# Performance work log

Measured on AMD Instinct MI355X. Metric: run time of the kernel, lower is better.

## Reference

```python
import jax, jax.numpy as jnp
import numpy as np

B, L, D = 2, 2048, 1024
H, HD = 16, 64   # num_heads, head_dim
LD = 256         # mla latent dim


def setup_inputs() -> dict:
    key = jax.random.key(0)
    ks = jax.random.split(key, 6)
    s = lambda fan_in: 1.0 / np.sqrt(fan_in)
    x_bld = jax.random.normal(ks[0], (B, L, D), dtype=jnp.float32)
    Wq = jax.random.normal(ks[1], (D, H, HD), dtype=jnp.float32) * s(D)
    Wkv_down = jax.random.normal(ks[2], (D, LD), dtype=jnp.float32) * s(D)
    Wk_up = jax.random.normal(ks[3], (LD, H, HD), dtype=jnp.float32) * s(LD)
    Wv_up = jax.random.normal(ks[4], (LD, H, HD), dtype=jnp.float32) * s(LD)
    Wout = jax.random.normal(ks[5], (H, HD, D), dtype=jnp.float32) * s(H * HD)
    return {"x_bld": x_bld, "Wq": Wq, "Wkv_down": Wkv_down,
            "Wk_up": Wk_up, "Wv_up": Wv_up, "Wout": Wout}


def reference(x_bld, Wq, Wkv_down, Wk_up, Wv_up, Wout):
    # projections
    q_blhd = jnp.einsum('bld,dhk->blhk', x_bld, Wq)
    latent_bll = jnp.einsum('bld,dc->blc', x_bld, Wkv_down)   # [B,L,LD]
    k_blhd = jnp.einsum('blc,chk->blhk', latent_bll, Wk_up)
    v_blhd = jnp.einsum('blc,chk->blhk', latent_bll, Wv_up)
    # attention scores [B,H,L,L]
    attn = jnp.einsum('bqhd,bkhd->bhqk', q_blhd, k_blhd) / jnp.sqrt(
        jnp.asarray(HD, dtype=x_bld.dtype))
    # causal mask (no window)
    l = x_bld.shape[1]
    mask = (jnp.arange(l)[None, :] <= jnp.arange(l)[:, None])[None, None]
    neg_inf = jnp.finfo(attn.dtype).min
    attn = jax.nn.softmax(jnp.where(mask, attn, neg_inf), axis=-1)
    y_blhd = jnp.einsum('bhqk,bkhd->bqhd', attn, v_blhd)
    return jnp.einsum('bqhd,hdo->bqo', y_blhd, Wout)
```

## Files before the change

### kernel.cpp

```cpp
#include <hip/hip_runtime.h>
#include <hip/hip_bf16.h>

#define BB   2
#define LL   2048
#define DD   1024
#define HH   16
#define HDD  64
#define LDIM 256
#define MTOT (BB * LL)

using short8  = __attribute__((ext_vector_type(8))) short;
using floatx4 = __attribute__((ext_vector_type(4))) float;

static __device__ __forceinline__ unsigned short f2bf(float x) {
  __hip_bfloat16 h = __float2bfloat16(x);
  return *reinterpret_cast<unsigned short*>(&h);
}
static __device__ __forceinline__ unsigned int pk_bf16(float a, float b) {
  return (unsigned int)f2bf(a) | ((unsigned int)f2bf(b) << 16);
}
static __device__ __forceinline__ void load_lds16(const unsigned short* g,
                                                  unsigned short* l) {
  __builtin_amdgcn_global_load_lds(
      (const __attribute__((address_space(1))) unsigned int*)g,
      (__attribute__((address_space(3))) unsigned int*)l, 16, 0, 0);
}
template <int N>
static __device__ __forceinline__ void waitcnt_vm() {
  if constexpr (N == 0) asm volatile("s_waitcnt vmcnt(0)" ::: "memory");
  else if constexpr (N == 2) asm volatile("s_waitcnt vmcnt(2)" ::: "memory");
  else if constexpr (N == 4) asm volatile("s_waitcnt vmcnt(4)" ::: "memory");
  else if constexpr (N == 6) asm volatile("s_waitcnt vmcnt(6)" ::: "memory");
  else if constexpr (N == 8) asm volatile("s_waitcnt vmcnt(8)" ::: "memory");
}
static __device__ __forceinline__ void lds_drain_barrier() {
  asm volatile("s_waitcnt lgkmcnt(0)\n\ts_barrier" ::: "memory");
}

__global__ __launch_bounds__(256) void cast_bf16(const float* __restrict__ in,
                                                 unsigned short* __restrict__ out,
                                                 int n4) {
  const int i = (blockIdx.x * 256 + threadIdx.x);
  if (i < n4) {
    float4 v = ((const float4*)in)[i];
    ushort4 o;
    o.x = f2bf(v.x); o.y = f2bf(v.y); o.z = f2bf(v.z); o.w = f2bf(v.w);
    ((ushort4*)out)[i] = o;
  }
}

__global__ __launch_bounds__(256) void transpose_cast5(
    const float* __restrict__ Wq, const float* __restrict__ Wkv,
    const float* __restrict__ Wku, const float* __restrict__ Wvu,
    const float* __restrict__ Wo,
    unsigned short* __restrict__ WqT, unsigned short* __restrict__ WkvT,
    unsigned short* __restrict__ WkuT, unsigned short* __restrict__ WvuT,
    unsigned short* __restrict__ WoT) {
  const float* src; unsigned short* dst; int R, C;
  switch (blockIdx.z) {
    case 0:  src = Wq;  dst = WqT;  R = 1024; C = 1024; break;
    case 1:  src = Wkv; dst = WkvT; R = 1024; C = 256;  break;
    case 2:  src = Wku; dst = WkuT; R = 256;  C = 1024; break;
    case 3:  src = Wvu; dst = WvuT; R = 256;  C = 1024; break;
    default: src = Wo;  dst = WoT;  R = 1024; C = 1024; break;
  }
  if ((int)blockIdx.x * 32 >= C || (int)blockIdx.y * 32 >= R) return;

  __shared__ float tile[32][33];
  const int tx = threadIdx.x, ty = threadIdx.y;
#pragma unroll
  for (int i = 0; i < 4; ++i) {
    const int r = blockIdx.y * 32 + ty + i * 8;
    tile[ty + i * 8][tx] = src[(size_t)r * C + blockIdx.x * 32 + tx];
  }
  __syncthreads();
#pragma unroll
  for (int i = 0; i < 4; ++i) {
    const int c = blockIdx.x * 32 + ty + i * 8;
    dst[(size_t)c * R + blockIdx.y * 32 + tx] = f2bf(tile[tx][ty + i * 8]);
  }
}

template <int KIND, int BMT, int BNT, int BKT>
__global__ __launch_bounds__(256) void gemm2(const unsigned short* __restrict__ A,
                                             const unsigned short* __restrict__ Bt0,
                                             const unsigned short* __restrict__ Bt1,
                                             void* __restrict__ C0,
                                             void* __restrict__ C1,
                                             int M, int N, int K, int nsplit) {
  constexpr int IM = BMT / 32, JN = BNT / 32;
  constexpr int TA = BMT * BKT, TB = BNT * BKT;
  constexpr int NIA = TA / 2048, NIB = TB / 2048;
  constexpr int NLD = NIA + NIB;
  constexpr int RPI = 2048 / BKT;
  __shared__ __align__(16) unsigned short As[2 * TA];
  __shared__ __align__(16) unsigned short Bs[2 * TB];

  const int tid  = threadIdx.x;
  const int w    = tid >> 6;
  const int lane = tid & 63;
  const int lo   = lane & 15;
  const int g    = lane >> 4;
  const int wr   = w >> 1, wc = w & 1;
  const int row0  = blockIdx.x * BMT;
  const int col0g = blockIdx.y * BNT;
  const bool second = (col0g >= nsplit);
  const unsigned short* Btp = second ? Bt1 : Bt0;
  const int col0 = second ? col0g - nsplit : col0g;

  floatx4 acc[IM][JN];
#pragma unroll
  for (int i = 0; i < IM; ++i)
#pragma unroll
    for (int j = 0; j < JN; ++j) acc[i][j] = (floatx4){0.f, 0.f, 0.f, 0.f};

  const int sr = (BKT == 32) ? (tid >> 2) : (tid >> 3);
  const int sc = (BKT == 32) ? (tid & 3) : (tid & 7);

  auto swz = [](int chunk, int row) {
    if constexpr (BKT == 32) return chunk ^ ((row >> 1) & 3);
    else                     return chunk ^ (row & 7);
  };

  auto stage = [&](int buf, int k0) {
#pragma unroll
    for (int inst = 0; inst < NIA; ++inst) {
      const int r  = inst * RPI + sr;
      const int cs = swz(sc, r);
      load_lds16(A + (size_t)(row0 + r) * K + k0 + cs * 8,
                 As + buf * TA + inst * 2048 + w * 512);
    }
#pragma unroll
    for (int inst = 0; inst < NIB; ++inst) {
      const int r  = inst * RPI + sr;
      const int cs = swz(sc, r);
      load_lds16(Btp + (size_t)(col0 + r) * K + k0 + cs * 8,
                 Bs + buf * TB + inst * 2048 + w * 512);
    }
  };

  const int nk = K / BKT;
  stage(0, 0);
  for (int it = 0; it < nk; ++it) {
    const int cur = it & 1;
    if (it + 1 < nk) {
      stage(cur ^ 1, (it + 1) * BKT);
      waitcnt_vm<NLD>();
    } else {
      waitcnt_vm<0>();
    }
    asm volatile("s_barrier" ::: "memory");

    const unsigned short* Ac = As + cur * TA;
    const unsigned short* Bc = Bs + cur * TB;
#pragma unroll
    for (int kk = 0; kk < BKT / 32; ++kk) {
      short8 af[IM], bf[JN];
#pragma unroll
      for (int i = 0; i < IM; ++i) {
        const int rm = (BMT / 2) * wr + 16 * i + lo;
        af[i] = *(const short8*)(Ac + (size_t)rm * BKT + swz(kk * 4 + g, rm) * 8);
      }
#pragma unroll
      for (int j = 0; j < JN; ++j) {
        const int rn = (BNT / 2) * wc + 16 * j + lo;
        bf[j] = *(const short8*)(Bc + (size_t)rn * BKT + swz(kk * 4 + g, rn) * 8);
      }
#pragma unroll
      for (int i = 0; i < IM; ++i)
#pragma unroll
        for (int j = 0; j < JN; ++j)
          acc[i][j] = __builtin_amdgcn_mfma_f32_16x16x32_bf16(af[i], bf[j], acc[i][j], 0, 0, 0);
    }

    lds_drain_barrier();
  }

#pragma unroll
  for (int i = 0; i < IM; ++i) {
    const int mbase = row0 + (BMT / 2) * wr + 16 * i + g * 4;
#pragma unroll
    for (int j = 0; j < JN; ++j) {
      const int nl = col0 + (BNT / 2) * wc + 16 * j + lo;
      const int bq = mbase >> 11, hh = nl >> 6, d = nl & 63;
      if (KIND == 2 && second) {
        const int l = mbase & 2047;
        uint2 o;
        o.x = pk_bf16(acc[i][j][0], acc[i][j][1]);
        o.y = pk_bf16(acc[i][j][2], acc[i][j][3]);
        *(uint2*)(&((unsigned short*)C1)[((size_t)(bq * HH + hh) * HDD + d) * LL + l]) = o;
      } else {
#pragma unroll
        for (int r = 0; r < 4; ++r) {
          const float v = acc[i][j][r];
          const int mm = mbase + r;
          const int l = mm & 2047;
          if (KIND == 0) {
            ((float*)C0)[(size_t)mm * N + nl] = v;
          } else if (KIND == 1) {
            if (!second)
              ((unsigned short*)C0)[((size_t)(bq * HH + hh) * LL + l) * HDD + d] = f2bf(v);
            else
              ((unsigned short*)C1)[(size_t)mm * LDIM + nl] = f2bf(v);
          } else {
            ((unsigned short*)C0)[((size_t)(bq * HH + hh) * LL + l) * HDD + d] = f2bf(v);
          }
        }
      }
    }
  }
}

#define SC2 0.18033688011112042f

__global__ __launch_bounds__(512, 4) void flash_mfma11(const unsigned short* __restrict__ Qh,
                                                       const unsigned short* __restrict__ Kh,
                                                       const unsigned short* __restrict__ Vt,
                                                       unsigned short* __restrict__ y) {
  const int w    = threadIdx.x >> 6;
  const int lane = threadIdx.x & 63;
  const int lo   = lane & 15;
  const int g    = lane >> 4;
  const int kw   = w >> 2;
  const int wq   = w & 3;
  const int h    = blockIdx.x;
  const int b    = blockIdx.y;
  const int pair = blockIdx.z;
  const int qtH  = 31 - pair;
  const int qtL  = pair;

  __shared__ __align__(16) unsigned short Ks[3 * 64 * 64];
  __shared__ __align__(16) unsigned short Vs[3 * 64 * 64];
  __shared__ __align__(16) unsigned short Pq[8][2][16 * 32];

  const size_t bh = (size_t)(b * HH + h);
  const unsigned short* Qp = Qh + bh * LL * HDD;
  const unsigned short* Kp = Kh + bh * LL * HDD;
  const unsigned short* Vp = Vt + bh * (size_t)HDD * LL;
  unsigned short* PwH = Pq[w][0];
  unsigned short* PwL = Pq[w][1];

  const int qHw = qtH * 64 + wq * 16;
  const int qLw = qtL * 64 + wq * 16;

  short8 qfH0 = *(const short8*)(Qp + (size_t)(qHw + lo) * HDD + g * 8);
  short8 qfH1 = *(const short8*)(Qp + (size_t)(qHw + lo) * HDD + 32 + g * 8);
  short8 qfL0 = *(const short8*)(Qp + (size_t)(qLw + lo) * HDD + g * 8);
  short8 qfL1 = *(const short8*)(Qp + (size_t)(qLw + lo) * HDD + 32 + g * 8);

  floatx4 otH[4], otL[4];
#pragma unroll
  for (int ds = 0; ds < 4; ++ds) {
    otH[ds] = (floatx4){0.f, 0.f, 0.f, 0.f};
    otL[ds] = (floatx4){0.f, 0.f, 0.f, 0.f};
  }
  float lsumH = 0.f, lsumL = 0.f;

  const int srow = lane >> 3;
  const int sch  = lane & 7;

  auto stage = [&](int buf, int k0) {
    const int row = w * 8 + srow;
    const int cs  = sch ^ (row & 7);
    load_lds16(Kp + (size_t)(k0 + row) * HDD + cs * 8, Ks + buf * 4096 + w * 512);
    load_lds16(Vp + (size_t)row * LL + k0 + cs * 8,    Vs + buf * 4096 + w * 512);
  };

  auto qk2 = [&](const unsigned short* Kc, bool doL, floatx4* stH, floatx4* stL) {
#pragma unroll
    for (int ks = 0; ks < 2; ++ks) {
      const int rm = kw * 32 + ks * 16 + lo;
      short8 a0 = *(const short8*)(Kc + rm * 64 + ((g ^ (rm & 7)) * 8));
      short8 a1 = *(const short8*)(Kc + rm * 64 + (((4 + g) ^ (rm & 7)) * 8));
      floatx4 s = (floatx4){0.f, 0.f, 0.f, 0.f};
      s = __builtin_amdgcn_mfma_f32_16x16x32_bf16(a0, qfH0, s, 0, 0, 0);
      s = __builtin_amdgcn_mfma_f32_16x16x32_bf16(a1, qfH1, s, 0, 0, 0);
      stH[ks] = s;
      if (doL) {
        floatx4 t = (floatx4){0.f, 0.f, 0.f, 0.f};
        t = __builtin_amdgcn_mfma_f32_16x16x32_bf16(a0, qfL0, t, 0, 0, 0);
        t = __builtin_amdgcn_mfma_f32_16x16x32_bf16(a1, qfL1, t, 0, 0, 0);
        stL[ks] = t;
      }
    }
  };
  auto sm = [&](floatx4* st, unsigned short* P, float& lsum, int qw, int k0,
                bool masked) {
    if (!masked) {
#pragma unroll
      for (int ks = 0; ks < 2; ++ks) {
        float p[4];
#pragma unroll
        for (int r = 0; r < 4; ++r) {
          p[r] = __builtin_amdgcn_exp2f(st[ks][r] * SC2);
          lsum += p[r];
        }
        uint2 w2;
        w2.x = pk_bf16(p[0], p[1]);
        w2.y = pk_bf16(p[2], p[3]);
        *(uint2*)(P + lo * 32 + (((ks * 2 + (g >> 1)) ^ (lo & 3)) * 8) + (g & 1) * 4) = w2;
      }
    } else {
      const int qq = qw + lo;
#pragma unroll
      for (int ks = 0; ks < 2; ++ks) {
        float p[4];
#pragma unroll
        for (int r = 0; r < 4; ++r) {
          const int kk = k0 + kw * 32 + ks * 16 + g * 4 + r;
          const float e = __builtin_amdgcn_exp2f(st[ks][r] * SC2);
          p[r] = (kk <= qq) ? e : 0.f;
          lsum += p[r];
        }
        uint2 w2;
        w2.x = pk_bf16(p[0], p[1]);
        w2.y = pk_bf16(p[2], p[3]);
        *(uint2*)(P + lo * 32 + (((ks * 2 + (g >> 1)) ^ (lo & 3)) * 8) + (g & 1) * 4) = w2;
      }
    }
  };
  auto pv2 = [&](const unsigned short* Vc, bool doL) {
    short8 pfH = *(const short8*)(PwH + lo * 32 + ((g ^ (lo & 3)) * 8));
    short8 pfL;
    if (doL) pfL = *(const short8*)(PwL + lo * 32 + ((g ^ (lo & 3)) * 8));
#pragma unroll
    for (int ds = 0; ds < 4; ++ds) {
      const int rm = ds * 16 + lo;
      short8 v = *(const short8*)(Vc + rm * 64 + (((kw * 4 + g) ^ (rm & 7)) * 8));
      otH[ds] = __builtin_amdgcn_mfma_f32_16x16x32_bf16(v, pfH, otH[ds], 0, 0, 0);
      if (doL)
        otL[ds] = __builtin_amdgcn_mfma_f32_16x16x32_bf16(v, pfL, otL[ds], 0, 0, 0);
    }
  };

  const int ntiles = qtH + 1;
  stage(0, 0);
  stage(1, 64);
  for (int it = 0; it < ntiles; ++it) {
    const int cur = it % 3;
    const int k0  = it * 64;
    if (it + 2 < ntiles) {
      stage((it + 2) % 3, k0 + 128);
      waitcnt_vm<4>();
    } else if (it + 1 < ntiles) {
      waitcnt_vm<2>();
    } else {
      waitcnt_vm<0>();
    }
    asm volatile("s_barrier" ::: "memory");

    const unsigned short* Kc = Ks + cur * 4096;
    const unsigned short* Vc = Vs + cur * 4096;
    const bool doL = (it <= qtL);

    floatx4 stH[2], stL[2];
    qk2(Kc, doL, stH, stL);
    sm(stH, PwH, lsumH, qHw, k0, it == qtH);
    if (doL) sm(stL, PwL, lsumL, qLw, k0, it == qtL);
    pv2(Vc, doL);

    lds_drain_barrier();
  }

  float sH = lsumH; sH += __shfl_xor(sH, 16); sH += __shfl_xor(sH, 32);
  float sL = lsumL; sL += __shfl_xor(sL, 16); sL += __shfl_xor(sL, 32);
  float* oshH = (float*)Ks;
  float* oshL = (float*)Vs;
  float* lsh  = (float*)&Pq[0][0][0];

  if (kw == 1) {
    const int base = (wq * 64 + lane) * 16;
#pragma unroll
    for (int ds = 0; ds < 4; ++ds) {
      *(floatx4*)(oshH + base + ds * 4) = otH[ds];
      *(floatx4*)(oshL + base + ds * 4) = otL[ds];
    }
    if (lane < 16) {
      lsh[wq * 16 + lane]      = sH;
      lsh[64 + wq * 16 + lane] = sL;
    }
  }
  __syncthreads();
  if (kw == 0) {
    const int base = (wq * 64 + lane) * 16;
#pragma unroll
    for (int ds = 0; ds < 4; ++ds) {
      otH[ds] += *(const floatx4*)(oshH + base + ds * 4);
      otL[ds] += *(const floatx4*)(oshL + base + ds * 4);
    }
    sH += lsh[wq * 16 + lo];
    sL += lsh[64 + wq * 16 + lo];

    auto finish = [&](floatx4* ot, float stot, int qw) {
      const float inv = 1.0f / stot;
#pragma unroll
      for (int ds = 0; ds < 4; ++ds) {
        uint2 o;
        o.x = pk_bf16(ot[ds][0] * inv, ot[ds][1] * inv);
        o.y = pk_bf16(ot[ds][2] * inv, ot[ds][3] * inv);
        *(uint2*)(y + (size_t)(b * LL + qw + lo) * (HH * HDD) + h * HDD + ds * 16 + g * 4) = o;
      }
    };
    finish(otH, sH, qHw);
    finish(otL, sL, qLw);
  }
}

extern "C" void kernel_launch(void* const* d_in, const int* in_sizes, int n_in,
                              void* d_out, int out_size, void* d_ws, size_t ws_size,
                              hipStream_t stream) {
  const float* x   = (const float*)d_in[0];
  const float* Wq  = (const float*)d_in[1];
  const float* Wkv = (const float*)d_in[2];
  const float* Wku = (const float*)d_in[3];
  const float* Wvu = (const float*)d_in[4];
  const float* Wo  = (const float*)d_in[5];
  float* out = (float*)d_out;

  unsigned short* xb     = (unsigned short*)d_ws;
  unsigned short* WqT    = xb + (size_t)MTOT * DD;
  unsigned short* WkvT   = WqT + 1024 * 1024;
  unsigned short* WkuT   = WkvT + 256 * 1024;
  unsigned short* WvuT   = WkuT + 1024 * 256;
  unsigned short* WoT    = WvuT + 1024 * 256;
  unsigned short* latent = WoT + 1024 * 1024;
  unsigned short* Qh     = latent + (size_t)MTOT * LDIM;
  unsigned short* Kh     = Qh + (size_t)MTOT * DD;
  unsigned short* Vt     = Kh + (size_t)MTOT * DD;
  unsigned short* y      = Vt + (size_t)MTOT * DD;

  cast_bf16<<<dim3(MTOT * DD / 1024), dim3(256), 0, stream>>>(x, xb, MTOT * DD / 4);
  transpose_cast5<<<dim3(32, 32, 5), dim3(32, 8), 0, stream>>>(
      Wq, Wkv, Wku, Wvu, Wo, WqT, WkvT, WkuT, WvuT, WoT);

  gemm2<1, 128, 64, 64><<<dim3(MTOT / 128, 1280 / 64), dim3(256), 0, stream>>>(
      xb, WqT, WkvT, Qh, latent, MTOT, 1280, DD, 1024);
  gemm2<2, 128, 128, 64><<<dim3(MTOT / 128, 2048 / 128), dim3(256), 0, stream>>>(
      latent, WkuT, WvuT, Kh, Vt, MTOT, 2048, LDIM, 1024);

  flash_mfma11<<<dim3(HH, BB, 16), dim3(512), 0, stream>>>(Qh, Kh, Vt, y);

  gemm2<0, 128, 64, 64><<<dim3(MTOT / 128, DD / 64), dim3(256), 0, stream>>>(
      y, WoT, nullptr, out, nullptr, MTOT, DD, DD, DD);
}
```

Baseline: 163.9 us.

## Process two KV tiles per barrier with a four-deep LDS ring

```diff
diff --git a/kernel.cpp b/kernel.cpp
--- a/kernel.cpp
+++ b/kernel.cpp
@@ -213,7 +213,7 @@
 
 #define SC2 0.18033688011112042f
 
-__global__ __launch_bounds__(512, 4) void flash_mfma11(const unsigned short* __restrict__ Qh,
+__global__ __launch_bounds__(512, 4) void flash_mfma12(const unsigned short* __restrict__ Qh,
                                                        const unsigned short* __restrict__ Kh,
                                                        const unsigned short* __restrict__ Vt,
                                                        unsigned short* __restrict__ y) {
@@ -229,8 +229,8 @@
   const int qtH  = 31 - pair;
   const int qtL  = pair;
 
-  __shared__ __align__(16) unsigned short Ks[3 * 64 * 64];
-  __shared__ __align__(16) unsigned short Vs[3 * 64 * 64];
+  __shared__ __align__(16) unsigned short Ks[4 * 64 * 64];
+  __shared__ __align__(16) unsigned short Vs[4 * 64 * 64];
   __shared__ __align__(16) unsigned short Pq[8][2][16 * 32];
 
   const size_t bh = (size_t)(b * HH + h);
@@ -266,7 +266,15 @@
     load_lds16(Vp + (size_t)row * LL + k0 + cs * 8,    Vs + buf * 4096 + w * 512);
   };
 
-  auto qk2 = [&](const unsigned short* Kc, bool doL, floatx4* stH, floatx4* stL) {
+  auto tile_body = [&](int it, int buf) {
+    const unsigned short* Kc = Ks + buf * 4096;
+    const unsigned short* Vc = Vs + buf * 4096;
+    const int k0  = it * 64;
+    const bool doL = (it <= qtL);
+    const bool mH  = (it == qtH);
+    const bool mL  = (it == qtL);
+
+    floatx4 stH[2], stL[2];
 #pragma unroll
     for (int ks = 0; ks < 2; ++ks) {
       const int rm = kw * 32 + ks * 16 + lo;
@@ -283,43 +291,45 @@
         stL[ks] = t;
       }
     }
-  };
-  auto sm = [&](floatx4* st, unsigned short* P, float& lsum, int qw, int k0,
-                bool masked) {
-    if (!masked) {
-#pragma unroll
-      for (int ks = 0; ks < 2; ++ks) {
-        float p[4];
-#pragma unroll
-        for (int r = 0; r < 4; ++r) {
-          p[r] = __builtin_amdgcn_exp2f(st[ks][r] * SC2);
-          lsum += p[r];
+
+    auto sm = [&](floatx4* st, unsigned short* P, float& lsum, int qw,
+                  bool masked) {
+      if (!masked) {
+#pragma unroll
+        for (int ks = 0; ks < 2; ++ks) {
+          float p[4];
+#pragma unroll
+          for (int r = 0; r < 4; ++r) {
+            p[r] = __builtin_amdgcn_exp2f(st[ks][r] * SC2);
+            lsum += p[r];
+          }
+          uint2 w2;
+          w2.x = pk_bf16(p[0], p[1]);
+          w2.y = pk_bf16(p[2], p[3]);
+          *(uint2*)(P + lo * 32 + (((ks * 2 + (g >> 1)) ^ (lo & 3)) * 8) + (g & 1) * 4) = w2;
         }
-        uint2 w2;
-        w2.x = pk_bf16(p[0], p[1]);
-        w2.y = pk_bf16(p[2], p[3]);
-        *(uint2*)(P + lo * 32 + (((ks * 2 + (g >> 1)) ^ (lo & 3)) * 8) + (g & 1) * 4) = w2;
-      }
-    } else {
-      const int qq = qw + lo;
-#pragma unroll
-      for (int ks = 0; ks < 2; ++ks) {
-        float p[4];
-#pragma unroll
-        for (int r = 0; r < 4; ++r) {
-          const int kk = k0 + kw * 32 + ks * 16 + g * 4 + r;
-          const float e = __builtin_amdgcn_exp2f(st[ks][r] * SC2);
-          p[r] = (kk <= qq) ? e : 0.f;
-          lsum += p[r];
+      } else {
+        const int qq = qw + lo;
+#pragma unroll
+        for (int ks = 0; ks < 2; ++ks) {
+          float p[4];
+#pragma unroll
+          for (int r = 0; r < 4; ++r) {
+            const int kk = k0 + kw * 32 + ks * 16 + g * 4 + r;
+            const float e = __builtin_amdgcn_exp2f(st[ks][r] * SC2);
+            p[r] = (kk <= qq) ? e : 0.f;
+            lsum += p[r];
+          }
+          uint2 w2;
+          w2.x = pk_bf16(p[0], p[1]);
+          w2.y = pk_bf16(p[2], p[3]);
+          *(uint2*)(P + lo * 32 + (((ks * 2 + (g >> 1)) ^ (lo & 3)) * 8) + (g & 1) * 4) = w2;
         }
-        uint2 w2;
-        w2.x = pk_bf16(p[0], p[1]);
-        w2.y = pk_bf16(p[2], p[3]);
-        *(uint2*)(P + lo * 32 + (((ks * 2 + (g >> 1)) ^ (lo & 3)) * 8) + (g & 1) * 4) = w2;
-      }
-    }
-  };
-  auto pv2 = [&](const unsigned short* Vc, bool doL) {
+      }
+    };
+    sm(stH, PwH, lsumH, qHw, mH);
+    if (doL) sm(stL, PwL, lsumL, qLw, mL);
+
     short8 pfH = *(const short8*)(PwH + lo * 32 + ((g ^ (lo & 3)) * 8));
     short8 pfL;
     if (doL) pfL = *(const short8*)(PwL + lo * 32 + ((g ^ (lo & 3)) * 8));
@@ -334,31 +344,31 @@
   };
 
   const int ntiles = qtH + 1;
-  stage(0, 0);
-  stage(1, 64);
-  for (int it = 0; it < ntiles; ++it) {
-    const int cur = it % 3;
-    const int k0  = it * 64;
-    if (it + 2 < ntiles) {
-      stage((it + 2) % 3, k0 + 128);
-      waitcnt_vm<4>();
-    } else if (it + 1 < ntiles) {
-      waitcnt_vm<2>();
-    } else {
-      waitcnt_vm<0>();
-    }
+  const int np  = ntiles >> 1;
+  const bool odd = (ntiles & 1);
+
+  stage(0, 0); stage(1, 64); stage(2, 128); stage(3, 192);
+
+  for (int j = 0; j < np; ++j) {
+    const int t0 = 2 * j;
+    if (j + 1 < np)      waitcnt_vm<4>();
+    else if (odd)        waitcnt_vm<2>();
+    else                 waitcnt_vm<0>();
     asm volatile("s_barrier" ::: "memory");
 
-    const unsigned short* Kc = Ks + cur * 4096;
-    const unsigned short* Vc = Vs + cur * 4096;
-    const bool doL = (it <= qtL);
-
-    floatx4 stH[2], stL[2];
-    qk2(Kc, doL, stH, stL);
-    sm(stH, PwH, lsumH, qHw, k0, it == qtH);
-    if (doL) sm(stL, PwL, lsumL, qLw, k0, it == qtL);
-    pv2(Vc, doL);
-
+    tile_body(t0,     t0 & 3);
+    tile_body(t0 + 1, (t0 + 1) & 3);
+
+    lds_drain_barrier();
+    const int tp = t0 + 4;
+    if (tp < ntiles)     stage(tp & 3, tp * 64);
+    if (tp + 1 < ntiles) stage((tp + 1) & 3, (tp + 1) * 64);
+  }
+  if (odd) {
+    const int t = ntiles - 1;
+    waitcnt_vm<0>();
+    asm volatile("s_barrier" ::: "memory");
+    tile_body(t, t & 3);
     lds_drain_barrier();
   }
 
@@ -438,7 +448,7 @@
   gemm2<2, 128, 128, 64><<<dim3(MTOT / 128, 2048 / 128), dim3(256), 0, stream>>>(
       latent, WkuT, WvuT, Kh, Vt, MTOT, 2048, LDIM, 1024);
 
-  flash_mfma11<<<dim3(HH, BB, 16), dim3(512), 0, stream>>>(Qh, Kh, Vt, y);
+  flash_mfma12<<<dim3(HH, BB, 16), dim3(512), 0, stream>>>(Qh, Kh, Vt, y);
 
   gemm2<0, 128, 64, 64><<<dim3(MTOT / 128, DD / 64), dim3(256), 0, stream>>>(
       y, WoT, nullptr, out, nullptr, MTOT, DD, DD, DD);
```

Result: no change. 162.5 us (-0.9%).
